# Performance work log

Measured on AMD Instinct MI355X. Metric: run time of the kernel, lower is better.

The kernel has to match this reference:

```python
import jax, jax.numpy as jnp
import numpy as np

WH, WW = 14, 14
NUM_HEADS = 12
NUM_REL = (2 * WH - 1) * (2 * WW - 1) + 3  # 732


def _gen_rel_pos_index(wh, ww):
    # Faithful numpy port of gen_relative_position_index (static, host-side)
    area = wh * ww
    coords = np.stack(np.meshgrid(np.arange(wh), np.arange(ww), indexing='ij'))  # (2, wh, ww)
    cf = coords.reshape(2, -1)  # (2, area)
    rel = cf[:, :, None] - cf[:, None, :]  # (2, area, area)
    rel = rel.transpose(1, 2, 0).copy()  # (area, area, 2)
    rel[..., 0] += wh - 1
    rel[..., 1] += ww - 1
    rel[..., 0] *= 2 * ww - 1
    nrd = (2 * wh - 1) * (2 * ww - 1) + 3
    idx = np.zeros((area + 1, area + 1), dtype=np.int64)
    idx[1:, 1:] = rel.sum(-1)
    idx[0, 0:] = nrd - 3
    idx[0:, 0] = nrd - 2
    idx[0, 0] = nrd - 1
    return idx


REL_IDX = jnp.asarray(_gen_rel_pos_index(WH, WW))  # (197, 197) int


def setup_inputs() -> dict:
    key = jax.random.key(0)
    k0, k1, k2, k3 = jax.random.split(key, 4)
    B, N, C = 64, WH * WW + 1, 768
    x = jax.random.normal(k0, (B, N, C), jnp.float32)
    qkv_w = jax.random.normal(k1, (3 * C, C), jnp.float32) * 0.02
    q_bias = jnp.zeros((C,), jnp.float32)
    k_bias = jnp.zeros((C,), jnp.float32)  # non-trainable buffer, always zeros
    v_bias = jnp.zeros((C,), jnp.float32)
    rel_table = jax.random.normal(k2, (NUM_REL, NUM_HEADS), jnp.float32) * 0.02
    proj_w = jax.random.normal(k3, (C, C), jnp.float32) * 0.02
    proj_b = jnp.zeros((C,), jnp.float32)
    return {"x": x, "qkv_w": qkv_w, "q_bias": q_bias, "k_bias": k_bias,
            "v_bias": v_bias, "rel_table": rel_table, "proj_w": proj_w, "proj_b": proj_b}


def reference(x, qkv_w, q_bias, k_bias, v_bias, rel_table, proj_w, proj_b):
    B, N, C = x.shape
    H = NUM_HEADS
    D = C // H
    scale = D ** -0.5
    # fused qkv projection with concatenated (q, k(zero), v) bias
    qkv_bias = jnp.concatenate([q_bias, k_bias, v_bias])
    qkv = x @ qkv_w.T + qkv_bias  # (B, N, 3C)
    qkv = qkv.reshape(B, N, 3, H, D).transpose(2, 0, 3, 1, 4)  # (3, B, H, N, D)
    q, k, v = qkv[0], qkv[1], qkv[2]
    # scores + gathered relative position bias
    attn = jnp.einsum('bhnd,bhmd->bhnm', q * scale, k)  # (B, H, N, N)
    rpb = rel_table[REL_IDX].transpose(2, 0, 1)  # (H, N, N)
    attn = jax.nn.softmax(attn + rpb[None], axis=-1)
    out = jnp.einsum('bhnm,bhmd->bhnd', attn, v)  # (B, H, N, D)
    out = out.transpose(0, 2, 1, 3).reshape(B, N, C)
    return out @ proj_w.T + proj_b
```

## Files before the change

### kernel.cpp

```cpp
#include <hip/hip_runtime.h>
#include <math.h>

#define B_   64
#define N_   197
#define C_   768
#define H_   12
#define D_   64
#define BN   12608
#define BN_PAD 12672
#define QKV_ELEMS 9682944
#define SCALE 0.125f
#define STRV 80
#define TPAD 72

typedef unsigned short ushort_t;
using bf16x8  = __attribute__((ext_vector_type(8))) __bf16;
using floatx4 = __attribute__((ext_vector_type(4))) float;
using ushort8 = __attribute__((ext_vector_type(8))) unsigned short;

__device__ __forceinline__ ushort_t f2bf(float f) {
    union { float f; unsigned u; } v; v.f = f;
    unsigned r = v.u + 0x7FFF + ((v.u >> 16) & 1);
    return (ushort_t)(r >> 16);
}

__device__ __forceinline__ float bf2f(ushort_t u) {
    union { unsigned u; float f; } v; v.u = ((unsigned)u) << 16;
    return v.f;
}

__device__ __forceinline__ void gload_lds16(const void* g, void* l) {
    __builtin_amdgcn_global_load_lds(
        (const __attribute__((address_space(1))) unsigned*)g,
        (__attribute__((address_space(3))) unsigned*)l, 16, 0, 0);
}

__device__ __forceinline__ int xcd_chunk(int orig, int nwg) {
    const int q = nwg >> 3, r = nwg & 7;
    const int x = orig & 7, i = orig >> 3;
    const int base = (x < r) ? x * (q + 1) : r * (q + 1) + (x - r) * q;
    return base + i;
}

__global__ __launch_bounds__(256) void cvt_all(
    const float* __restrict__ x,  const float* __restrict__ w1,
    const float* __restrict__ w2,
    ushort_t* __restrict__ xb, ushort_t* __restrict__ wb,
    ushort_t* __restrict__ pwb)
{
    const int i = blockIdx.x * 256 + threadIdx.x;
    const float* s; ushort_t* d; int j;
    if (i < 2420736)      { s = x;  d = xb;  j = i; }
    else if (i < 2863104) { s = w1; d = wb;  j = i - 2420736; }
    else                  { s = w2; d = pwb; j = i - 2863104; }
    float4 v = ((const float4*)s)[j];
    ushort4 o;
    o.x = f2bf(v.x); o.y = f2bf(v.y); o.z = f2bf(v.z); o.w = f2bf(v.w);
    ((ushort4*)d)[j] = o;
}

__global__ __launch_bounds__(256) void build_rpb(
    const float* __restrict__ rel_table,
    ushort_t* __restrict__ t4)
{
    const int p = blockIdx.x * 256 + threadIdx.x;
    if (p >= 4 * 197 * TPAD) return;
    const int nl = p % TPAD;
    const int rest = p / TPAD;
    const int m = rest % 197, rt = rest / 197;
    const int n = rt * 64 + nl;
    const bool valid = (n < 197);
    int idx = 0;
    if (valid) {
        if (n == 0 && m == 0)      idx = 731;
        else if (n == 0)           idx = 729;
        else if (m == 0)           idx = 730;
        else {
            const int pp = n - 1, qq = m - 1;
            idx = (pp / 14 - qq / 14 + 13) * 27 + (pp % 14 - qq % 14 + 13);
        }
    }
#pragma unroll
    for (int h = 0; h < 12; ++h)
        t4[((size_t)(rt * 12 + h) * 197 + m) * TPAD + nl] =
            valid ? f2bf(rel_table[idx * 12 + h]) : (ushort_t)0;
}

__global__ __launch_bounds__(256, 4) void qkv_gemm_mfma(
    const ushort_t* __restrict__ xb,
    const ushort_t* __restrict__ wb,
    const float* __restrict__ qb,
    const float* __restrict__ kb,
    const float* __restrict__ vb,
    ushort_t* __restrict__ qkvb)
{
    __shared__ ushort_t lA[128 * 64];
    __shared__ ushort_t lB[128 * 64];
    const int t = threadIdx.x;
    const int w = t >> 6, lane = t & 63;
    const int quad = lane >> 4, li = lane & 15;
    const int wm = w >> 1, wn = w & 1;
    const int f = xcd_chunk(blockIdx.y * 18 + blockIdx.x, 18 * 99);
    const int o0 = (f % 18) * 128, m0 = (f / 18) * 128;

    floatx4 acc[4][4];
#pragma unroll
    for (int i = 0; i < 4; ++i)
#pragma unroll
        for (int j = 0; j < 4; ++j) acc[i][j] = (floatx4)0.f;

    const int rloc = lane >> 3;
    const int gdma = (lane & 7) ^ rloc;
    const int rx   = li & 7;

    for (int kt = 0; kt < 12; ++kt) {
        const int k0 = kt * 64;
#pragma unroll
        for (int s = 0; s < 4; ++s) {
            const int rb = w * 32 + s * 8;
            gload_lds16(xb + ((size_t)(m0 + rb + rloc)) * 768 + k0 + gdma * 8,
                        &lA[rb * 64]);
            gload_lds16(wb + ((size_t)(o0 + rb + rloc)) * 768 + k0 + gdma * 8,
                        &lB[rb * 64]);
        }
        __syncthreads();
#pragma unroll
        for (int kk = 0; kk < 2; ++kk) {
            bf16x8 af[4], bfr[4];
#pragma unroll
            for (int mi = 0; mi < 4; ++mi)
                af[mi] = *(const bf16x8*)
                    &lA[(wm * 64 + mi * 16 + li) * 64 + ((kk * 4 + quad) ^ rx) * 8];
#pragma unroll
            for (int ni = 0; ni < 4; ++ni)
                bfr[ni] = *(const bf16x8*)
                    &lB[(wn * 64 + ni * 16 + li) * 64 + ((kk * 4 + quad) ^ rx) * 8];
#pragma unroll
            for (int mi = 0; mi < 4; ++mi)
#pragma unroll
                for (int ni = 0; ni < 4; ++ni)
                    acc[mi][ni] = __builtin_amdgcn_mfma_f32_16x16x32_bf16(
                        af[mi], bfr[ni], acc[mi][ni], 0, 0, 0);
        }
        __syncthreads();
    }

    const int which = o0 / 768;
    const float* bias = (which == 0) ? qb : ((which == 1) ? kb : vb);
    ushort_t* dst = qkvb + (size_t)which * QKV_ELEMS;
    const float sc = (which == 0) ? SCALE : 1.0f;

#pragma unroll
    for (int mi = 0; mi < 4; ++mi) {
#pragma unroll
        for (int r = 0; r < 4; ++r) {
            const int m = m0 + wm * 64 + mi * 16 + quad * 4 + r;
            if (m < BN) {
                const int b = m / 197, n = m % 197;
#pragma unroll
                for (int ni = 0; ni < 4; ++ni) {
                    const int o  = o0 + wn * 64 + ni * 16 + li;
                    const int ol = o - which * 768;
                    const int h = ol >> 6, d = ol & 63;
                    dst[(((size_t)b * 12 + h) * 197 + n) * 64 + d] =
                        f2bf((acc[mi][ni][r] + bias[ol]) * sc);
                }
            }
        }
    }
}

__global__ __launch_bounds__(256, 4) void attn_mfma(
    const ushort_t* __restrict__ qkvb,
    const ushort_t* __restrict__ t4,
    ushort_t* __restrict__ aout)
{
    __shared__ ushort_t Qs[64 * TPAD];
    __shared__ ushort_t Ks[64 * 64];
    __shared__ ushort_t Vt[64 * STRV];
    __shared__ ushort_t Ps[64 * STRV];

    const int f = xcd_chunk(blockIdx.y * 4 + blockIdx.x, 4 * 768);
    const int rt = f & 3, bh = f >> 2;
    const int h = bh % 12, bb = bh / 12;
    const int t = threadIdx.x;
    const int w = t >> 6, lane = t & 63, quad = lane >> 4, li = lane & 15;
    const size_t base = (size_t)bh * (197 * 64);
    const ushort_t* Qg = qkvb + base;
    const ushort_t* Kg = qkvb + (size_t)QKV_ELEMS + base;
    const ushort_t* Vg = qkvb + (size_t)2 * QKV_ELEMS + base;
    const int r0 = rt * 64;
    const ushort_t* slab = t4 + (size_t)(rt * 12 + h) * (197 * TPAD);

    {
        const int rloc = lane >> 3, g = (lane & 7) ^ rloc;
#pragma unroll
        for (int s = 0; s < 2; ++s) {
            const int rb = (w * 2 + s) * 8;
            gload_lds16(Qg + (size_t)(r0 + rb + rloc) * 64 + g * 8, &Qs[rb * 64]);
        }
    }

    int nrow[4];
#pragma unroll
    for (int r = 0; r < 4; ++r) nrow[r] = r0 + w * 16 + quad * 4 + r;

    float m_run[4], l_run[4];
    floatx4 accO[4];
#pragma unroll
    for (int r = 0; r < 4; ++r) { m_run[r] = -INFINITY; l_run[r] = 0.f; }
#pragma unroll
    for (int dt = 0; dt < 4; ++dt) accO[dt] = (floatx4)0.f;

    __syncthreads();

    bf16x8 aq0, aq1;
    {
        const int rq = w * 16 + li, rxq = rq & 7;
        aq0 = *(const bf16x8*)&Qs[rq * 64 + (quad ^ rxq) * 8];
        aq1 = *(const bf16x8*)&Qs[rq * 64 + ((4 + quad) ^ rxq) * 8];
    }
    __syncthreads();

    for (int cc = 0; cc < 4; ++cc) {
        {
            const int rloc = lane >> 3, g = (lane & 7) ^ rloc;
#pragma unroll
            for (int s = 0; s < 2; ++s) {
                const int rb = (w * 2 + s) * 8;
                gload_lds16(Kg + (size_t)(cc * 64 + rb + rloc) * 64 + g * 8,
                            &Ks[rb * 64]);
            }
        }
        for (int c = w; c < 9; c += 4)
            gload_lds16(slab + (size_t)cc * 4608 + c * 512 + lane * 8,
                        &Qs[c * 512]);
        {
            const int c = lane;
            const int mg = cc * 64 + c;
            ushort8 v0, v1;
            if (mg < 197) {
                v0 = *(const ushort8*)(Vg + (size_t)mg * 64 + w * 16);
                v1 = *(const ushort8*)(Vg + (size_t)mg * 64 + w * 16 + 8);
            } else {
                v0 = (ushort8)(unsigned short)0; v1 = v0;
            }
#pragma unroll
            for (int j = 0; j < 8; ++j) Vt[(w * 16 + j) * STRV + c] = v0[j];
#pragma unroll
            for (int j = 0; j < 8; ++j) Vt[(w * 16 + 8 + j) * STRV + c] = v1[j];
        }
        __syncthreads();

        floatx4 sacc[4];
#pragma unroll
        for (int tl = 0; tl < 4; ++tl) {
            const int rk = tl * 16 + li, rxk = rk & 7;
            bf16x8 bk0 = *(const bf16x8*)&Ks[rk * 64 + (quad ^ rxk) * 8];
            bf16x8 bk1 = *(const bf16x8*)&Ks[rk * 64 + ((4 + quad) ^ rxk) * 8];
            floatx4 sa = (floatx4)0.f;
            sa = __builtin_amdgcn_mfma_f32_16x16x32_bf16(aq0, bk0, sa, 0, 0, 0);
            sa = __builtin_amdgcn_mfma_f32_16x16x32_bf16(aq1, bk1, sa, 0, 0, 0);
            sacc[tl] = sa;
        }

#pragma unroll
        for (int tl = 0; tl < 4; ++tl) {
            const int mg = cc * 64 + tl * 16 + li;
            if (mg >= 197) {
#pragma unroll
                for (int r = 0; r < 4; ++r) sacc[tl][r] = -INFINITY;
            } else {
                ushort4 bv = *(const ushort4*)
                    &Qs[(tl * 16 + li) * TPAD + w * 16 + quad * 4];
                sacc[tl][0] += bf2f(bv.x);
                sacc[tl][1] += bf2f(bv.y);
                sacc[tl][2] += bf2f(bv.z);
                sacc[tl][3] += bf2f(bv.w);
            }
        }

#pragma unroll
        for (int r = 0; r < 4; ++r) {
            float mx = fmaxf(fmaxf(sacc[0][r], sacc[1][r]),
                             fmaxf(sacc[2][r], sacc[3][r]));
            mx = fmaxf(mx, __shfl_xor(mx, 1));
            mx = fmaxf(mx, __shfl_xor(mx, 2));
            mx = fmaxf(mx, __shfl_xor(mx, 4));
            mx = fmaxf(mx, __shfl_xor(mx, 8));
            const float mnew = fmaxf(m_run[r], mx);
            const float alpha = __expf(m_run[r] - mnew);
            m_run[r] = mnew;
            const float p0 = __expf(sacc[0][r] - mnew);
            const float p1 = __expf(sacc[1][r] - mnew);
            const float p2 = __expf(sacc[2][r] - mnew);
            const float p3 = __expf(sacc[3][r] - mnew);
            float rs = p0 + p1 + p2 + p3;
            rs += __shfl_xor(rs, 1);
            rs += __shfl_xor(rs, 2);
            rs += __shfl_xor(rs, 4);
            rs += __shfl_xor(rs, 8);
            l_run[r] = l_run[r] * alpha + rs;
#pragma unroll
            for (int dt = 0; dt < 4; ++dt) accO[dt][r] *= alpha;
            const int prow = w * 16 + quad * 4 + r;
            Ps[prow * STRV +  0 + li] = f2bf(p0);
            Ps[prow * STRV + 16 + li] = f2bf(p1);
            Ps[prow * STRV + 32 + li] = f2bf(p2);
            Ps[prow * STRV + 48 + li] = f2bf(p3);
        }

        {
            const int rp = w * 16 + li;
            bf16x8 pa0 = *(const bf16x8*)&Ps[rp * STRV + 0  + quad * 8];
            bf16x8 pa1 = *(const bf16x8*)&Ps[rp * STRV + 32 + quad * 8];
#pragma unroll
            for (int dt = 0; dt < 4; ++dt) {
                const int rv = dt * 16 + li;
                bf16x8 bv0 = *(const bf16x8*)&Vt[rv * STRV + 0  + quad * 8];
                bf16x8 bv1 = *(const bf16x8*)&Vt[rv * STRV + 32 + quad * 8];
                accO[dt] = __builtin_amdgcn_mfma_f32_16x16x32_bf16(
                    pa0, bv0, accO[dt], 0, 0, 0);
                accO[dt] = __builtin_amdgcn_mfma_f32_16x16x32_bf16(
                    pa1, bv1, accO[dt], 0, 0, 0);
            }
        }
        __syncthreads();
    }

#pragma unroll
    for (int r = 0; r < 4; ++r) {
        const int n = nrow[r];
        if (n < 197) {
            const float inv = 1.0f / l_run[r];
            ushort_t* op = aout + ((size_t)(bb * 197 + n)) * 768 + h * 64;
#pragma unroll
            for (int dt = 0; dt < 4; ++dt)
                op[dt * 16 + li] = f2bf(accO[dt][r] * inv);
        }
    }
}

__global__ __launch_bounds__(256, 4) void proj_gemm_mfma(
    const ushort_t* __restrict__ ab,
    const ushort_t* __restrict__ wb,
    const float* __restrict__ bias,
    float* __restrict__ out)
{
    __shared__ ushort_t lA[128 * 64];
    __shared__ ushort_t lB[128 * 64];
    const int t = threadIdx.x;
    const int w = t >> 6, lane = t & 63;
    const int quad = lane >> 4, li = lane & 15;
    const int wm = w >> 1, wn = w & 1;
    const int f = xcd_chunk(blockIdx.y * 6 + blockIdx.x, 6 * 99);
    const int o0 = (f % 6) * 128, m0 = (f / 6) * 128;

    floatx4 acc[4][4];
#pragma unroll
    for (int i = 0; i < 4; ++i)
#pragma unroll
        for (int j = 0; j < 4; ++j) acc[i][j] = (floatx4)0.f;

    const int rloc = lane >> 3;
    const int gdma = (lane & 7) ^ rloc;
    const int rx   = li & 7;

    for (int kt = 0; kt < 12; ++kt) {
        const int k0 = kt * 64;
#pragma unroll
        for (int s = 0; s < 4; ++s) {
            const int rb = w * 32 + s * 8;
            gload_lds16(ab + ((size_t)(m0 + rb + rloc)) * 768 + k0 + gdma * 8,
                        &lA[rb * 64]);
            gload_lds16(wb + ((size_t)(o0 + rb + rloc)) * 768 + k0 + gdma * 8,
                        &lB[rb * 64]);
        }
        __syncthreads();
#pragma unroll
        for (int kk = 0; kk < 2; ++kk) {
            bf16x8 af[4], bfr[4];
#pragma unroll
            for (int mi = 0; mi < 4; ++mi)
                af[mi] = *(const bf16x8*)
                    &lA[(wm * 64 + mi * 16 + li) * 64 + ((kk * 4 + quad) ^ rx) * 8];
#pragma unroll
            for (int ni = 0; ni < 4; ++ni)
                bfr[ni] = *(const bf16x8*)
                    &lB[(wn * 64 + ni * 16 + li) * 64 + ((kk * 4 + quad) ^ rx) * 8];
#pragma unroll
            for (int mi = 0; mi < 4; ++mi)
#pragma unroll
                for (int ni = 0; ni < 4; ++ni)
                    acc[mi][ni] = __builtin_amdgcn_mfma_f32_16x16x32_bf16(
                        af[mi], bfr[ni], acc[mi][ni], 0, 0, 0);
        }
        __syncthreads();
    }

#pragma unroll
    for (int mi = 0; mi < 4; ++mi) {
#pragma unroll
        for (int r = 0; r < 4; ++r) {
            const int m = m0 + wm * 64 + mi * 16 + quad * 4 + r;
            if (m < BN) {
                float* op = out + (size_t)m * 768;
#pragma unroll
                for (int ni = 0; ni < 4; ++ni) {
                    const int o = o0 + wn * 64 + ni * 16 + li;
                    op[o] = acc[mi][ni][r] + bias[o];
                }
            }
        }
    }
}

extern "C" void kernel_launch(void* const* d_in, const int* in_sizes, int n_in,
                              void* d_out, int out_size, void* d_ws, size_t ws_size,
                              hipStream_t stream)
{
    const float* x         = (const float*)d_in[0];
    const float* qkv_w     = (const float*)d_in[1];
    const float* q_bias    = (const float*)d_in[2];
    const float* k_bias    = (const float*)d_in[3];
    const float* v_bias    = (const float*)d_in[4];
    const float* rel_table = (const float*)d_in[5];
    const float* proj_w    = (const float*)d_in[6];
    const float* proj_b    = (const float*)d_in[7];
    float* out = (float*)d_out;

    char* ws = (char*)d_ws;
    ushort_t* qkvb  = (ushort_t*)ws;
    ushort_t* xb    = (ushort_t*)(ws + 58097664);
    ushort_t* aoutb = xb;
    ushort_t* wb    = (ushort_t*)(ws + 77561856);
    ushort_t* t4b   = wb;
    ushort_t* pwb   = (ushort_t*)(ws + 81100800);

    cvt_all<<<11760, 256, 0, stream>>>(x, qkv_w, proj_w, xb, wb, pwb);

    dim3 g1(18, 99);
    qkv_gemm_mfma<<<g1, 256, 0, stream>>>(xb, wb, q_bias, k_bias, v_bias, qkvb);

    build_rpb<<<222, 256, 0, stream>>>(rel_table, t4b);

    dim3 g2(4, 768);
    attn_mfma<<<g2, 256, 0, stream>>>(qkvb, t4b, aoutb);

    dim3 g3(6, 99);
    proj_gemm_mfma<<<g3, 256, 0, stream>>>(aoutb, pwb, proj_b, out);
}
```

Before: 235.4 us.

## Replace online softmax with register-resident two-pass softmax in attention

The attention kernel now computes all QK^T score tiles for the full 197-key row up front and keeps them in registers (13 floatx4 tiles). It then does one exact max/sum softmax pass and runs the P·V loop afterwards. This removes the per-chunk running-max rescaling of the accumulators and the repeated exp/shuffle reductions. It also skips the K loads, bias-slab loads and MFMAs for fully padded key tiles in the last chunk. The cost is higher register pressure and an extra loop with extra barriers, plus stale P entries in the last chunk that rely on V being zero-padded.

New measurement: 224.4 us. 4.7% less time.

```diff
diff --git a/kernel.cpp b/kernel.cpp
--- a/kernel.cpp
+++ b/kernel.cpp
@@ -205,10 +205,7 @@
 #pragma unroll
     for (int r = 0; r < 4; ++r) nrow[r] = r0 + w * 16 + quad * 4 + r;
 
-    float m_run[4], l_run[4];
     floatx4 accO[4];
-#pragma unroll
-    for (int r = 0; r < 4; ++r) { m_run[r] = -INFINITY; l_run[r] = 0.f; }
 #pragma unroll
     for (int dt = 0; dt < 4; ++dt) accO[dt] = (floatx4)0.f;
 
@@ -222,19 +219,77 @@
     }
     __syncthreads();
 
+    floatx4 sv[13];
+#pragma unroll
     for (int cc = 0; cc < 4; ++cc) {
         {
             const int rloc = lane >> 3, g = (lane & 7) ^ rloc;
 #pragma unroll
             for (int s = 0; s < 2; ++s) {
                 const int rb = (w * 2 + s) * 8;
-                gload_lds16(Kg + (size_t)(cc * 64 + rb + rloc) * 64 + g * 8,
-                            &Ks[rb * 64]);
-            }
-        }
-        for (int c = w; c < 9; c += 4)
+                if (cc < 3 || rb < 16)
+                    gload_lds16(Kg + (size_t)(cc * 64 + rb + rloc) * 64 + g * 8,
+                                &Ks[rb * 64]);
+            }
+        }
+        for (int c = w; c < ((cc == 3) ? 3 : 9); c += 4)
             gload_lds16(slab + (size_t)cc * 4608 + c * 512 + lane * 8,
                         &Qs[c * 512]);
+        __syncthreads();
+
+#pragma unroll
+        for (int tl = 0; tl < 4; ++tl) {
+            if (cc < 3 || tl == 0) {
+                const int rk = tl * 16 + li, rxk = rk & 7;
+                bf16x8 bk0 = *(const bf16x8*)&Ks[rk * 64 + (quad ^ rxk) * 8];
+                bf16x8 bk1 = *(const bf16x8*)&Ks[rk * 64 + ((4 + quad) ^ rxk) * 8];
+                floatx4 sa = (floatx4)0.f;
+                sa = __builtin_amdgcn_mfma_f32_16x16x32_bf16(aq0, bk0, sa, 0, 0, 0);
+                sa = __builtin_amdgcn_mfma_f32_16x16x32_bf16(aq1, bk1, sa, 0, 0, 0);
+                const int mg = cc * 64 + tl * 16 + li;
+                if (mg >= 197) {
+#pragma unroll
+                    for (int r = 0; r < 4; ++r) sa[r] = -INFINITY;
+                } else {
+                    ushort4 bv = *(const ushort4*)
+                        &Qs[(tl * 16 + li) * TPAD + w * 16 + quad * 4];
+                    sa[0] += bf2f(bv.x);
+                    sa[1] += bf2f(bv.y);
+                    sa[2] += bf2f(bv.z);
+                    sa[3] += bf2f(bv.w);
+                }
+                sv[cc * 4 + tl] = sa;
+            }
+        }
+        __syncthreads();
+    }
+
+    float inv[4];
+#pragma unroll
+    for (int r = 0; r < 4; ++r) {
+        float mx = sv[0][r];
+#pragma unroll
+        for (int i = 1; i < 13; ++i) mx = fmaxf(mx, sv[i][r]);
+        mx = fmaxf(mx, __shfl_xor(mx, 1));
+        mx = fmaxf(mx, __shfl_xor(mx, 2));
+        mx = fmaxf(mx, __shfl_xor(mx, 4));
+        mx = fmaxf(mx, __shfl_xor(mx, 8));
+        float rs = 0.f;
+#pragma unroll
+        for (int i = 0; i < 13; ++i) {
+            const float p = __expf(sv[i][r] - mx);
+            sv[i][r] = p;
+            rs += p;
+        }
+        rs += __shfl_xor(rs, 1);
+        rs += __shfl_xor(rs, 2);
+        rs += __shfl_xor(rs, 4);
+        rs += __shfl_xor(rs, 8);
+        inv[r] = 1.0f / rs;
+    }
+
+#pragma unroll
+    for (int cc = 0; cc < 4; ++cc) {
         {
             const int c = lane;
             const int mg = cc * 64 + c;
@@ -250,65 +305,15 @@
 #pragma unroll
             for (int j = 0; j < 8; ++j) Vt[(w * 16 + 8 + j) * STRV + c] = v1[j];
         }
-        __syncthreads();
-
-        floatx4 sacc[4];
-#pragma unroll
-        for (int tl = 0; tl < 4; ++tl) {
-            const int rk = tl * 16 + li, rxk = rk & 7;
-            bf16x8 bk0 = *(const bf16x8*)&Ks[rk * 64 + (quad ^ rxk) * 8];
-            bf16x8 bk1 = *(const bf16x8*)&Ks[rk * 64 + ((4 + quad) ^ rxk) * 8];
-            floatx4 sa = (floatx4)0.f;
-            sa = __builtin_amdgcn_mfma_f32_16x16x32_bf16(aq0, bk0, sa, 0, 0, 0);
-            sa = __builtin_amdgcn_mfma_f32_16x16x32_bf16(aq1, bk1, sa, 0, 0, 0);
-            sacc[tl] = sa;
-        }
-
-#pragma unroll
-        for (int tl = 0; tl < 4; ++tl) {
-            const int mg = cc * 64 + tl * 16 + li;
-            if (mg >= 197) {
-#pragma unroll
-                for (int r = 0; r < 4; ++r) sacc[tl][r] = -INFINITY;
-            } else {
-                ushort4 bv = *(const ushort4*)
-                    &Qs[(tl * 16 + li) * TPAD + w * 16 + quad * 4];
-                sacc[tl][0] += bf2f(bv.x);
-                sacc[tl][1] += bf2f(bv.y);
-                sacc[tl][2] += bf2f(bv.z);
-                sacc[tl][3] += bf2f(bv.w);
-            }
-        }
-
 #pragma unroll
         for (int r = 0; r < 4; ++r) {
-            float mx = fmaxf(fmaxf(sacc[0][r], sacc[1][r]),
-                             fmaxf(sacc[2][r], sacc[3][r]));
-            mx = fmaxf(mx, __shfl_xor(mx, 1));
-            mx = fmaxf(mx, __shfl_xor(mx, 2));
-            mx = fmaxf(mx, __shfl_xor(mx, 4));
-            mx = fmaxf(mx, __shfl_xor(mx, 8));
-            const float mnew = fmaxf(m_run[r], mx);
-            const float alpha = __expf(m_run[r] - mnew);
-            m_run[r] = mnew;
-            const float p0 = __expf(sacc[0][r] - mnew);
-            const float p1 = __expf(sacc[1][r] - mnew);
-            const float p2 = __expf(sacc[2][r] - mnew);
-            const float p3 = __expf(sacc[3][r] - mnew);
-            float rs = p0 + p1 + p2 + p3;
-            rs += __shfl_xor(rs, 1);
-            rs += __shfl_xor(rs, 2);
-            rs += __shfl_xor(rs, 4);
-            rs += __shfl_xor(rs, 8);
-            l_run[r] = l_run[r] * alpha + rs;
-#pragma unroll
-            for (int dt = 0; dt < 4; ++dt) accO[dt][r] *= alpha;
             const int prow = w * 16 + quad * 4 + r;
-            Ps[prow * STRV +  0 + li] = f2bf(p0);
-            Ps[prow * STRV + 16 + li] = f2bf(p1);
-            Ps[prow * STRV + 32 + li] = f2bf(p2);
-            Ps[prow * STRV + 48 + li] = f2bf(p3);
-        }
+#pragma unroll
+            for (int tl = 0; tl < 4; ++tl)
+                if (cc < 3 || tl == 0)
+                    Ps[prow * STRV + tl * 16 + li] = f2bf(sv[cc * 4 + tl][r]);
+        }
+        __syncthreads();
 
         {
             const int rp = w * 16 + li;
@@ -332,11 +337,10 @@
     for (int r = 0; r < 4; ++r) {
         const int n = nrow[r];
         if (n < 197) {
-            const float inv = 1.0f / l_run[r];
             ushort_t* op = aout + ((size_t)(bb * 197 + n)) * 768 + h * 64;
 #pragma unroll
             for (int dt = 0; dt < 4; ++dt)
-                op[dt * 16 + li] = f2bf(accO[dt][r] * inv);
+                op[dt * 16 + li] = f2bf(accO[dt][r] * inv[r]);
         }
     }
 }
```
